# Optimization experiments

Hardware: AMD Instinct MI355X
Metric: run time of the kernel (lower is better)

The kernel has to match this reference:

```python
import jax, jax.numpy as jnp
import numpy as np

B = 1024
N_NODES = 30
E_PER = 82
IN_F = 128
HID = 256
HEADS = (3, 2, 1)
N_EH = 41


def _lin(k, fi, fo):
    s = 1.0 / np.sqrt(fi)
    kw, kb = jax.random.split(k)
    W = jax.random.uniform(kw, (fi, fo), jnp.float32, -s, s)
    b = jax.random.uniform(kb, (fo,), jnp.float32, -s, s)
    return W, b


def setup_inputs() -> dict:
    key = jax.random.key(0)
    ks = list(jax.random.split(key, 32))
    rng = np.random.default_rng(0)
    # base 30-node graph with E_PER directed edges, no self-loops
    src = rng.integers(0, N_NODES, E_PER)
    dst = (src + rng.integers(1, N_NODES, E_PER)) % N_NODES
    base = np.stack([src, dst])  # [2, E_PER]
    offs = (np.arange(B) * N_NODES)[None, None, :]  # [1,1,B]
    ei = (base[:, :, None] + offs).transpose(0, 2, 1).reshape(2, -1)  # [2, B*E_PER]
    e_h = rng.choice(E_PER, N_EH, replace=False)
    d = {}
    d["x"] = jax.random.normal(ks[0], (B * N_NODES, IN_F), jnp.float32)
    d["edge_index"] = jnp.asarray(ei, dtype=jnp.int32)
    d["e_h_pairs"] = jnp.asarray(base[:, e_h].T, dtype=jnp.int32)  # [N_EH, 2]
    d["Wp"], d["bp"] = _lin(ks[1], IN_F, HID)
    i = 2
    for l, H in enumerate(HEADS):
        d[f"ln_g{l}"] = jnp.ones((HID,), jnp.float32)
        d[f"ln_b{l}"] = jnp.zeros((HID,), jnp.float32)
        d[f"Wl{l}"], d[f"bl{l}"] = _lin(ks[i], HID, H * HID); i += 1
        d[f"Wr{l}"], d[f"br{l}"] = _lin(ks[i], HID, H * HID); i += 1
        d[f"att{l}"] = jax.random.normal(ks[i], (H, HID), jnp.float32) * 0.1; i += 1
        d[f"bias{l}"] = jnp.zeros((HID,), jnp.float32)
    dims = [2 * HID, 256, 128, 128, 1]
    for j in range(4):
        d[f"Wm{j}"], d[f"bm{j}"] = _lin(ks[i], dims[j], dims[j + 1]); i += 1
    return d


def _layer_norm(h, g, b):
    mu = jnp.mean(h, -1, keepdims=True)
    var = jnp.mean((h - mu) ** 2, -1, keepdims=True)
    return (h - mu) * jax.lax.rsqrt(var + 1e-5) * g + b


def _gatv2(h, src, dst, n, Wl, bl, Wr, br, att, bias):
    # PyG GATv2Conv, concat=False (mean over heads), self-loops already in src/dst
    H, C = att.shape
    xl = (h @ Wl + bl).reshape(-1, H, C)  # source transform
    xr = (h @ Wr + br).reshape(-1, H, C)  # target transform
    xj = xl[src]                          # [E,H,C]
    e = jax.nn.leaky_relu(xj + xr[dst], 0.2)
    logits = jnp.einsum('ehc,hc->eh', e, att)  # [E,H]
    m = jax.lax.stop_gradient(jax.ops.segment_max(logits, dst, num_segments=n))
    ex = jnp.exp(logits - m[dst])
    denom = jax.ops.segment_sum(ex, dst, num_segments=n)
    alpha = ex / denom[dst]               # softmax over incoming edges of dst
    out = jax.ops.segment_sum(xj * alpha[..., None], dst, num_segments=n)  # [N,H,C]
    return jnp.mean(out, 1) + bias


def reference(x, edge_index, e_h_pairs, Wp, bp,
              ln_g0, ln_b0, Wl0, bl0, Wr0, br0, att0, bias0,
              ln_g1, ln_b1, Wl1, bl1, Wr1, br1, att1, bias1,
              ln_g2, ln_b2, Wl2, bl2, Wr2, br2, att2, bias2,
              Wm0, bm0, Wm1, bm1, Wm2, bm2, Wm3, bm3):
    n = x.shape[0]
    loops = jnp.arange(n, dtype=edge_index.dtype)
    src = jnp.concatenate([edge_index[0], loops])
    dst = jnp.concatenate([edge_index[1], loops])
    lrelu = lambda v: jax.nn.leaky_relu(v, 0.01)
    h = x @ Wp + bp
    layers = [(ln_g0, ln_b0, Wl0, bl0, Wr0, br0, att0, bias0),
              (ln_g1, ln_b1, Wl1, bl1, Wr1, br1, att1, bias1),
              (ln_g2, ln_b2, Wl2, bl2, Wr2, br2, att2, bias2)]
    for (g, b, Wl, bl, Wr, br, att, bias) in layers:
        hn = _layer_norm(h, g, b)
        hc = _gatv2(hn, src, dst, n, Wl, bl, Wr, br, att, bias)
        h = lrelu(hc) + h  # dropout is identity in eval
    hb = h.reshape(-1, N_NODES, HID)  # [B, 30, 256]
    ef = jnp.concatenate([hb[:, e_h_pairs[:, 0], :], hb[:, e_h_pairs[:, 1], :]], -1)
    o = ef.reshape(-1, 2 * HID)
    o = lrelu(o @ Wm0 + bm0)
    o = lrelu(o @ Wm1 + bm1)
    o = lrelu(o @ Wm2 + bm2)
    o = o @ Wm3 + bm3
    return o.reshape(-1)
```

## Files before the change

### kernel.cpp

```cpp
#include <hip/hip_runtime.h>
#include <hip/hip_bf16.h>
#include <math.h>

#define N_NODES 30
#define E_BASE  82
#define E_TOT   112
#define B_GRAPH 1024
#define HID     256
#define NTOT    (B_GRAPH * N_NODES)
#define MAXIN   32
#define N_EH    41
#define M_MLP   (B_GRAPH * N_EH)

#define META_SRC  0
#define META_DST  E_TOT
#define META_CNT  (2 * E_TOT)
#define META_LIST 256
#define META_INTS 1216

typedef __attribute__((ext_vector_type(8))) short bf16x8;
typedef __attribute__((ext_vector_type(4))) short bf16x4;
typedef __attribute__((ext_vector_type(4))) float f32x4;
#define AS3 __attribute__((address_space(3)))
#define AS1 __attribute__((address_space(1)))

__device__ __forceinline__ void gload_lds16(const void* g, void* l) {
  __builtin_amdgcn_global_load_lds((const AS1 void*)g, (AS3 void*)l, 16, 0, 0);
}

__device__ __forceinline__ float b2f(short s) {
  union { unsigned u; float f; } x;
  x.u = ((unsigned)(unsigned short)s) << 16;
  return x.f;
}

__global__ void build_graph(const int* __restrict__ ei, int* __restrict__ meta) {
  __shared__ int cnt[N_NODES];
  int tid = threadIdx.x;
  if (tid < N_NODES) cnt[tid] = 0;
  __syncthreads();
  if (tid < E_TOT) {
    int s, d;
    if (tid < E_BASE) { s = ei[tid]; d = ei[B_GRAPH * E_BASE + tid]; }
    else              { s = tid - E_BASE; d = s; }
    meta[META_SRC + tid] = s;
    meta[META_DST + tid] = d;
    int pos = atomicAdd(&cnt[d], 1);
    if (pos < MAXIN) meta[META_LIST + d * MAXIN + pos] = tid;
  }
  __syncthreads();
  if (tid < N_NODES) meta[META_CNT + tid] = cnt[tid];
}

struct WtJob { const float* in; int K, N, tstart, ooff; };
struct WtArgs { WtJob j[10]; };

__global__ __launch_bounds__(256)
void transpose_weights(WtArgs args, __hip_bfloat16* __restrict__ out) {
  int b = blockIdx.x;
  int ji = 0;
  #pragma unroll
  for (int i = 1; i < 10; i++) if (b >= args.j[i].tstart) ji = i;
  WtJob jb = args.j[ji];
  int t = b - jb.tstart;
  int ntn = jb.N >> 5;
  int tk = t / ntn, tn = t - tk * ntn;
  int k0 = tk * 32, n0 = tn * 32;
  __shared__ float s[32][33];
  int tx = threadIdx.x & 31, ty = threadIdx.x >> 5;
  #pragma unroll
  for (int p = 0; p < 4; p++)
    s[ty + p * 8][tx] = jb.in[(size_t)(k0 + ty + p * 8) * jb.N + n0 + tx];
  __syncthreads();
  __hip_bfloat16* o = out + jb.ooff;
  #pragma unroll
  for (int p = 0; p < 4; p++) {
    int n = ty + p * 8;
    o[(size_t)(n0 + n) * jb.K + k0 + tx] = __float2bfloat16(s[tx][n]);
  }
}

template<int ACT, int OUTBF>
__global__ __launch_bounds__(256)
void gemm_mfma(const __hip_bfloat16* __restrict__ A, const __hip_bfloat16* __restrict__ Bt,
               const float* __restrict__ bias, const float* __restrict__ bias2,
               void* __restrict__ Cv, int M, int K, int N, int N1)
{
  __shared__ __hip_bfloat16 sA[128 * 32];
  __shared__ __hip_bfloat16 sB[128 * 32];
  const int tid = threadIdx.x;
  const int lane = tid & 63;
  const int wave = tid >> 6;
  const int wx = wave & 1, wy = wave >> 1;
  const int bm = blockIdx.x, bn = blockIdx.y;
  const int mrow = lane & 15, quad = lane >> 4;

  const int r0 = tid >> 2, kc0 = (tid & 3) * 8;
  const __hip_bfloat16* Ag0 = A + (size_t)(bm * 128 + r0) * K + kc0;
  const __hip_bfloat16* Ag1 = A + (size_t)(bm * 128 + r0 + 64) * K + kc0;
  const __hip_bfloat16* Bg0 = Bt + (size_t)(bn * 128 + r0) * K + kc0;
  const __hip_bfloat16* Bg1 = Bt + (size_t)(bn * 128 + r0 + 64) * K + kc0;

  f32x4 acc[4][4];
  #pragma unroll
  for (int i = 0; i < 4; i++)
    #pragma unroll
    for (int j = 0; j < 4; j++)
      acc[i][j] = (f32x4){0.f, 0.f, 0.f, 0.f};

  for (int kt = 0; kt < K; kt += 32) {
    __syncthreads();
    gload_lds16(Ag0 + kt, &sA[tid * 8]);
    gload_lds16(Ag1 + kt, &sA[2048 + tid * 8]);
    gload_lds16(Bg0 + kt, &sB[tid * 8]);
    gload_lds16(Bg1 + kt, &sB[2048 + tid * 8]);
    __syncthreads();

    bf16x8 af[4], bfr[4];
    #pragma unroll
    for (int i = 0; i < 4; i++) {
      af[i]  = *(const bf16x8*)&sA[(wy * 64 + i * 16 + mrow) * 32 + quad * 8];
      bfr[i] = *(const bf16x8*)&sB[(wx * 64 + i * 16 + mrow) * 32 + quad * 8];
    }
    #pragma unroll
    for (int i = 0; i < 4; i++)
      #pragma unroll
      for (int j = 0; j < 4; j++)
        acc[i][j] = __builtin_amdgcn_mfma_f32_16x16x32_bf16(af[i], bfr[j], acc[i][j], 0, 0, 0);
  }

  #pragma unroll
  for (int i = 0; i < 4; i++) {
    #pragma unroll
    for (int r = 0; r < 4; r++) {
      size_t row = (size_t)bm * 128 + wy * 64 + i * 16 + quad * 4 + r;
      #pragma unroll
      for (int j = 0; j < 4; j++) {
        int col = bn * 128 + wx * 64 + j * 16 + mrow;
        float bc = (col < N1) ? bias[col] : bias2[col - N1];
        float v = acc[i][j][r] + bc;
        if (ACT) v = v > 0.f ? v : 0.01f * v;
        if (OUTBF) ((__hip_bfloat16*)Cv)[row * N + col] = __float2bfloat16(v);
        else       ((float*)Cv)[row * N + col] = v;
      }
    }
  }
}

template<int ACT, int OUTBF>
__global__ __launch_bounds__(256)
void gemm_mfma_f32a(const float* __restrict__ A, const __hip_bfloat16* __restrict__ Bt,
                    const float* __restrict__ bias, void* __restrict__ Cv,
                    int M, int K, int N)
{
  __shared__ __hip_bfloat16 sA[128 * 32];
  __shared__ __hip_bfloat16 sB[128 * 32];
  const int tid = threadIdx.x;
  const int lane = tid & 63;
  const int wave = tid >> 6;
  const int wx = wave & 1, wy = wave >> 1;
  const int bm = blockIdx.x, bn = blockIdx.y;
  const int mrow = lane & 15, quad = lane >> 4;

  const int r0 = tid >> 2, kc0 = (tid & 3) * 8;
  const float* Ag0 = A + (size_t)(bm * 128 + r0) * K + kc0;
  const float* Ag1 = A + (size_t)(bm * 128 + r0 + 64) * K + kc0;
  const __hip_bfloat16* Bg0 = Bt + (size_t)(bn * 128 + r0) * K + kc0;
  const __hip_bfloat16* Bg1 = Bt + (size_t)(bn * 128 + r0 + 64) * K + kc0;

  f32x4 acc[4][4];
  #pragma unroll
  for (int i = 0; i < 4; i++)
    #pragma unroll
    for (int j = 0; j < 4; j++)
      acc[i][j] = (f32x4){0.f, 0.f, 0.f, 0.f};

  for (int kt = 0; kt < K; kt += 32) {
    float4 a00 = *(const float4*)(Ag0 + kt);
    float4 a01 = *(const float4*)(Ag0 + kt + 4);
    float4 a10 = *(const float4*)(Ag1 + kt);
    float4 a11 = *(const float4*)(Ag1 + kt + 4);
    __syncthreads();
    {
      __hip_bfloat16 t[8];
      t[0] = __float2bfloat16(a00.x); t[1] = __float2bfloat16(a00.y);
      t[2] = __float2bfloat16(a00.z); t[3] = __float2bfloat16(a00.w);
      t[4] = __float2bfloat16(a01.x); t[5] = __float2bfloat16(a01.y);
      t[6] = __float2bfloat16(a01.z); t[7] = __float2bfloat16(a01.w);
      *(bf16x8*)&sA[tid * 8] = *(bf16x8*)t;
      t[0] = __float2bfloat16(a10.x); t[1] = __float2bfloat16(a10.y);
      t[2] = __float2bfloat16(a10.z); t[3] = __float2bfloat16(a10.w);
      t[4] = __float2bfloat16(a11.x); t[5] = __float2bfloat16(a11.y);
      t[6] = __float2bfloat16(a11.z); t[7] = __float2bfloat16(a11.w);
      *(bf16x8*)&sA[2048 + tid * 8] = *(bf16x8*)t;
    }
    gload_lds16(Bg0 + kt, &sB[tid * 8]);
    gload_lds16(Bg1 + kt, &sB[2048 + tid * 8]);
    __syncthreads();

    bf16x8 af[4], bfr[4];
    #pragma unroll
    for (int i = 0; i < 4; i++) {
      af[i]  = *(const bf16x8*)&sA[(wy * 64 + i * 16 + mrow) * 32 + quad * 8];
      bfr[i] = *(const bf16x8*)&sB[(wx * 64 + i * 16 + mrow) * 32 + quad * 8];
    }
    #pragma unroll
    for (int i = 0; i < 4; i++)
      #pragma unroll
      for (int j = 0; j < 4; j++)
        acc[i][j] = __builtin_amdgcn_mfma_f32_16x16x32_bf16(af[i], bfr[j], acc[i][j], 0, 0, 0);
  }

  #pragma unroll
  for (int i = 0; i < 4; i++) {
    #pragma unroll
    for (int r = 0; r < 4; r++) {
      size_t row = (size_t)bm * 128 + wy * 64 + i * 16 + quad * 4 + r;
      #pragma unroll
      for (int j = 0; j < 4; j++) {
        int col = bn * 128 + wx * 64 + j * 16 + mrow;
        float v = acc[i][j][r] + bias[col];
        if (ACT) v = v > 0.f ? v : 0.01f * v;
        if (OUTBF) ((__hip_bfloat16*)Cv)[row * N + col] = __float2bfloat16(v);
        else       ((float*)Cv)[row * N + col] = v;
      }
    }
  }
}

__global__ __launch_bounds__(256)
void gemm_mfma_pair(const float* __restrict__ h, const int* __restrict__ pairs,
                    const __hip_bfloat16* __restrict__ Bt, const float* __restrict__ bias,
                    __hip_bfloat16* __restrict__ C, int N)
{
  const int K = 512;
  __shared__ __hip_bfloat16 sA[128 * 32];
  __shared__ __hip_bfloat16 sB[128 * 32];
  const int tid = threadIdx.x;
  const int lane = tid & 63;
  const int wave = tid >> 6;
  const int wx = wave & 1, wy = wave >> 1;
  const int bm = blockIdx.x, bn = blockIdx.y;
  const int mrow = lane & 15, quad = lane >> 4;

  const float* pu[2]; const float* pv[2]; int sub[2];
  #pragma unroll
  for (int cI = 0; cI < 2; cI++) {
    int c = tid + cI * 256;
    int r0 = c >> 2; sub[cI] = (c & 3) * 8;
    int R = bm * 128 + r0;
    int b = R / N_EH, p = R - b * N_EH;
    int u = pairs[p * 2], v = pairs[p * 2 + 1];
    pu[cI] = h + ((size_t)b * N_NODES + u) * HID;
    pv[cI] = h + ((size_t)b * N_NODES + v) * HID;
  }

  const int r0 = tid >> 2, kc0 = (tid & 3) * 8;
  const __hip_bfloat16* Bg0 = Bt + (size_t)(bn * 128 + r0) * K + kc0;
  const __hip_bfloat16* Bg1 = Bt + (size_t)(bn * 128 + r0 + 64) * K + kc0;

  f32x4 acc[4][4];
  #pragma unroll
  for (int i = 0; i < 4; i++)
    #pragma unroll
    for (int j = 0; j < 4; j++)
      acc[i][j] = (f32x4){0.f, 0.f, 0.f, 0.f};

  for (int kt = 0; kt < K; kt += 32) {
    float4 av[2][2];
    #pragma unroll
    for (int cI = 0; cI < 2; cI++) {
      const float* src = (kt < 256 ? pu[cI] + kt : pv[cI] + kt - 256) + sub[cI];
      av[cI][0] = *(const float4*)src;
      av[cI][1] = *(const float4*)(src + 4);
    }
    __syncthreads();
    #pragma unroll
    for (int cI = 0; cI < 2; cI++) {
      __hip_bfloat16 t[8];
      t[0] = __float2bfloat16(av[cI][0].x); t[1] = __float2bfloat16(av[cI][0].y);
      t[2] = __float2bfloat16(av[cI][0].z); t[3] = __float2bfloat16(av[cI][0].w);
      t[4] = __float2bfloat16(av[cI][1].x); t[5] = __float2bfloat16(av[cI][1].y);
      t[6] = __float2bfloat16(av[cI][1].z); t[7] = __float2bfloat16(av[cI][1].w);
      *(bf16x8*)&sA[(tid + cI * 256) * 8] = *(bf16x8*)t;
    }
    gload_lds16(Bg0 + kt, &sB[tid * 8]);
    gload_lds16(Bg1 + kt, &sB[2048 + tid * 8]);
    __syncthreads();

    bf16x8 af[4], bfr[4];
    #pragma unroll
    for (int i = 0; i < 4; i++) {
      af[i]  = *(const bf16x8*)&sA[(wy * 64 + i * 16 + mrow) * 32 + quad * 8];
      bfr[i] = *(const bf16x8*)&sB[(wx * 64 + i * 16 + mrow) * 32 + quad * 8];
    }
    #pragma unroll
    for (int i = 0; i < 4; i++)
      #pragma unroll
      for (int j = 0; j < 4; j++)
        acc[i][j] = __builtin_amdgcn_mfma_f32_16x16x32_bf16(af[i], bfr[j], acc[i][j], 0, 0, 0);
  }

  #pragma unroll
  for (int i = 0; i < 4; i++) {
    #pragma unroll
    for (int r = 0; r < 4; r++) {
      size_t row = (size_t)bm * 128 + wy * 64 + i * 16 + quad * 4 + r;
      #pragma unroll
      for (int j = 0; j < 4; j++) {
        int col = bn * 128 + wx * 64 + j * 16 + mrow;
        float v = acc[i][j][r] + bias[col];
        v = v > 0.f ? v : 0.01f * v;
        C[row * N + col] = __float2bfloat16(v);
      }
    }
  }
}

__global__ __launch_bounds__(256)
void layernorm(const float* __restrict__ h, const float* __restrict__ g,
               const float* __restrict__ b, __hip_bfloat16* __restrict__ hn)
{
  const int wv = threadIdx.x >> 6, lane = threadIdx.x & 63;
  const size_t row = (size_t)blockIdx.x * 4 + wv;
  const float* hr = h + row * HID;
  float v[4];
  float sum = 0.f;
  #pragma unroll
  for (int j = 0; j < 4; j++) { v[j] = hr[lane + 64 * j]; sum += v[j]; }
  #pragma unroll
  for (int off = 32; off; off >>= 1) sum += __shfl_xor(sum, off);
  float mu = sum * (1.f / 256.f);
  float vs = 0.f;
  #pragma unroll
  for (int j = 0; j < 4; j++) { float d = v[j] - mu; vs += d * d; }
  #pragma unroll
  for (int off = 32; off; off >>= 1) vs += __shfl_xor(vs, off);
  float rs = rsqrtf(vs * (1.f / 256.f) + 1e-5f);
  __hip_bfloat16* outr = hn + row * HID;
  #pragma unroll
  for (int j = 0; j < 4; j++) {
    int c = lane + 64 * j;
    outr[c] = __float2bfloat16((v[j] - mu) * rs * g[c] + b[c]);
  }
}

__global__ __launch_bounds__(256)
void gat_alpha(const __hip_bfloat16* __restrict__ xcat,
               const float* __restrict__ att, float* __restrict__ alphaG,
               const int* __restrict__ meta, int H)
{
  __shared__ __hip_bfloat16 sxl[N_NODES * HID];
  __shared__ __hip_bfloat16 sxr[N_NODES * HID];
  __shared__ float slog[E_TOT];
  __shared__ float smax[N_NODES];
  __shared__ float sden[N_NODES];
  __shared__ int ssrc[E_TOT], sdst[E_TOT], scnt[N_NODES], slist[N_NODES * MAXIN];

  const int tid = threadIdx.x;
  const int g = blockIdx.x, hh = blockIdx.y;
  const size_t nodebase = (size_t)g * N_NODES;
  const int S = 2 * H * HID;

  {
    int i = tid;
    #pragma unroll
    for (int p = 0; p < 4; p++, i += 256) {
      if (i < N_NODES * HID / 8) {
        int node = i >> 5, c = (i & 31) * 8;
        const __hip_bfloat16* row = &xcat[(nodebase + node) * S + c];
        gload_lds16(row + hh * HID, &sxl[(size_t)i * 8]);
        gload_lds16(row + (H + hh) * HID, &sxr[(size_t)i * 8]);
      }
    }
  }

  if (tid < E_TOT) { ssrc[tid] = meta[META_SRC + tid]; sdst[tid] = meta[META_DST + tid]; }
  if (tid < N_NODES) { scnt[tid] = meta[META_CNT + tid]; sden[tid] = 0.f; }
  for (int i = tid; i < N_NODES * MAXIN; i += 256) slist[i] = meta[META_LIST + i];

  const int wv = tid >> 6, l32 = tid & 31, esub = (tid >> 5) & 1;
  const int c0 = l32 * 8;
  float attr[8];
  #pragma unroll
  for (int j = 0; j < 8; j++) attr[j] = att[hh * HID + c0 + j];
  __syncthreads();

  #pragma unroll
  for (int pass = 0; pass < 14; pass++) {
    int e = pass * 8 + wv * 2 + esub;
    bf16x8 a = *(const bf16x8*)&sxl[ssrc[e] * HID + c0];
    bf16x8 b = *(const bf16x8*)&sxr[sdst[e] * HID + c0];
    float sum = 0.f;
    #pragma unroll
    for (int j = 0; j < 8; j++) {
      float v = b2f(a[j]) + b2f(b[j]);
      v = v > 0.f ? v : 0.2f * v;
      sum += v * attr[j];
    }
    #pragma unroll
    for (int off = 16; off; off >>= 1) sum += __shfl_xor(sum, off);
    if (l32 == 0) slog[e] = sum;
  }
  __syncthreads();

  if (tid < N_NODES) {
    int cnt = scnt[tid];
    const int* lst = &slist[tid * MAXIN];
    float m = -1e30f;
    for (int i = 0; i < cnt; i++) m = fmaxf(m, slog[lst[i]]);
    smax[tid] = m;
  }
  __syncthreads();
  if (tid < E_TOT) {
    float ex = expf(slog[tid] - smax[sdst[tid]]);
    slog[tid] = ex;
    atomicAdd(&sden[sdst[tid]], ex);
  }
  __syncthreads();
  if (tid < E_TOT)
    alphaG[((size_t)g * H + hh) * E_TOT + tid] = slog[tid] / sden[sdst[tid]];
}

template<int DO_LN>
__global__ __launch_bounds__(256, 4)
void gat_agg(const __hip_bfloat16* __restrict__ xcat, const float* __restrict__ alphaG,
             const float* __restrict__ bias, float* __restrict__ h,
             const float* __restrict__ lnG, const float* __restrict__ lnB,
             __hip_bfloat16* __restrict__ hn, const int* __restrict__ meta, int H)
{
  __shared__ __hip_bfloat16 sxl[2][N_NODES * HID];
  __shared__ float salpha[2][E_TOT];
  __shared__ int ssrc[E_TOT], scnt[N_NODES], slist[N_NODES * MAXIN];

  const int tid = threadIdx.x;
  const int g = blockIdx.x;
  const size_t nodebase = (size_t)g * N_NODES;
  const int S = 2 * H * HID;
  const int c4 = tid & 63;
  const int ng = tid >> 6;

  if (tid < E_TOT) ssrc[tid] = meta[META_SRC + tid];
  if (tid < N_NODES) scnt[tid] = meta[META_CNT + tid];
  for (int i = tid; i < N_NODES * MAXIN; i += 256) slist[i] = meta[META_LIST + i];

  float4 hres[8];
  #pragma unroll
  for (int ki = 0; ki < 8; ki++) {
    int k = ng + ki * 4;
    if (k < N_NODES) hres[ki] = *(const float4*)&h[(nodebase + k) * HID + c4 * 4];
  }

  {
    int i = tid;
    #pragma unroll
    for (int p = 0; p < 4; p++, i += 256) {
      if (i < N_NODES * HID / 8) {
        int node = i >> 5, c = (i & 31) * 8;
        gload_lds16(&xcat[(nodebase + node) * S + 0 * HID + c], &sxl[0][(size_t)i * 8]);
      }
    }
    if (tid < E_TOT) salpha[0][tid] = alphaG[((size_t)g * H + 0) * E_TOT + tid];
  }

  float acc[8][4];
  #pragma unroll
  for (int ki = 0; ki < 8; ki++)
    #pragma unroll
    for (int j = 0; j < 4; j++) acc[ki][j] = 0.f;

  for (int hh = 0; hh < H; hh++) {
    const int buf = hh & 1;
    __syncthreads();
    if (hh + 1 < H) {
      const int nb = buf ^ 1;
      int i = tid;
      #pragma unroll
      for (int p = 0; p < 4; p++, i += 256) {
        if (i < N_NODES * HID / 8) {
          int node = i >> 5, c = (i & 31) * 8;
          gload_lds16(&xcat[(nodebase + node) * S + (hh + 1) * HID + c], &sxl[nb][(size_t)i * 8]);
        }
      }
      if (tid < E_TOT) salpha[nb][tid] = alphaG[((size_t)g * H + hh + 1) * E_TOT + tid];
    }
    #pragma unroll
    for (int ki = 0; ki < 8; ki++) {
      int k = ng + ki * 4;
      if (k < N_NODES) {
        int cnt = scnt[k];
        const int* lst = &slist[k * MAXIN];
        for (int i = 0; i < cnt; i++) {
          int e = lst[i];
          float al = salpha[buf][e];
          bf16x4 v = *(const bf16x4*)&sxl[buf][ssrc[e] * HID + c4 * 4];
          acc[ki][0] += al * b2f(v[0]);
          acc[ki][1] += al * b2f(v[1]);
          acc[ki][2] += al * b2f(v[2]);
          acc[ki][3] += al * b2f(v[3]);
        }
      }
    }
  }

  const float invH = 1.f / (float)H;
  const float4 bs = *(const float4*)&bias[c4 * 4];
  float4 gv, bv;
  if (DO_LN) {
    gv = *(const float4*)&lnG[c4 * 4];
    bv = *(const float4*)&lnB[c4 * 4];
  }
  #pragma unroll
  for (int ki = 0; ki < 8; ki++) {
    int k = ng + ki * 4;
    if (k < N_NODES) {
      float o0 = acc[ki][0] * invH + bs.x; o0 = o0 > 0.f ? o0 : 0.01f * o0; o0 += hres[ki].x;
      float o1 = acc[ki][1] * invH + bs.y; o1 = o1 > 0.f ? o1 : 0.01f * o1; o1 += hres[ki].y;
      float o2 = acc[ki][2] * invH + bs.z; o2 = o2 > 0.f ? o2 : 0.01f * o2; o2 += hres[ki].z;
      float o3 = acc[ki][3] * invH + bs.w; o3 = o3 > 0.f ? o3 : 0.01f * o3; o3 += hres[ki].w;
      float4 o4 = {o0, o1, o2, o3};
      *(float4*)&h[(nodebase + k) * HID + c4 * 4] = o4;
      if (DO_LN) {
        float sum = o0 + o1 + o2 + o3;
        #pragma unroll
        for (int off = 32; off; off >>= 1) sum += __shfl_xor(sum, off);
        float mu = sum * (1.f / 256.f);
        float d0 = o0 - mu, d1 = o1 - mu, d2 = o2 - mu, d3 = o3 - mu;
        float vs = d0 * d0 + d1 * d1 + d2 * d2 + d3 * d3;
        #pragma unroll
        for (int off = 32; off; off >>= 1) vs += __shfl_xor(vs, off);
        float rs = rsqrtf(vs * (1.f / 256.f) + 1e-5f);
        __hip_bfloat16 t[4];
        t[0] = __float2bfloat16(d0 * rs * gv.x + bv.x);
        t[1] = __float2bfloat16(d1 * rs * gv.y + bv.y);
        t[2] = __float2bfloat16(d2 * rs * gv.z + bv.z);
        t[3] = __float2bfloat16(d3 * rs * gv.w + bv.w);
        *(bf16x4*)&hn[(nodebase + k) * HID + c4 * 4] = *(bf16x4*)t;
      }
    }
  }
}

__global__ __launch_bounds__(256)
void mlp_out(const float* __restrict__ o3, const float* __restrict__ w,
             const float* __restrict__ b3, float* __restrict__ out)
{
  const int wv = threadIdx.x >> 6, lane = threadIdx.x & 63;
  const int row = blockIdx.x * 4 + wv;
  const float* orow = o3 + (size_t)row * 128;
  float s = orow[lane] * w[lane] + orow[lane + 64] * w[lane + 64];
  #pragma unroll
  for (int off = 32; off; off >>= 1) s += __shfl_xor(s, off);
  if (lane == 0) out[row] = s + b3[0];
}

extern "C" void kernel_launch(void* const* d_in, const int* in_sizes, int n_in,
                              void* d_out, int out_size, void* d_ws, size_t ws_size,
                              hipStream_t stream) {
  const float* x     = (const float*)d_in[0];
  const int*   ei    = (const int*)d_in[1];
  const int*   pairs = (const int*)d_in[2];
  const float* bp    = (const float*)d_in[4];
  const float *lng[3], *lnb[3], *bl[3], *br[3], *att[3], *bias[3];
  const float *WlF[3], *WrF[3];
  for (int l = 0; l < 3; l++) {
    int base = 5 + l * 8;
    lng[l]  = (const float*)d_in[base + 0];
    lnb[l]  = (const float*)d_in[base + 1];
    WlF[l]  = (const float*)d_in[base + 2];
    bl[l]   = (const float*)d_in[base + 3];
    WrF[l]  = (const float*)d_in[base + 4];
    br[l]   = (const float*)d_in[base + 5];
    att[l]  = (const float*)d_in[base + 6];
    bias[l] = (const float*)d_in[base + 7];
  }
  const float* WmF[4] = {(const float*)d_in[29], (const float*)d_in[31],
                         (const float*)d_in[33], (const float*)d_in[35]};
  const float* bm[4] = {(const float*)d_in[30], (const float*)d_in[32],
                        (const float*)d_in[34], (const float*)d_in[36]};

  float* ws  = (float*)d_ws;
  float* h   = ws;
  __hip_bfloat16* hnb = (__hip_bfloat16*)(ws + 7864320);
  __hip_bfloat16* xcat = (__hip_bfloat16*)(ws + 11796480);
  float* alphaG = ws + 35389440;
  __hip_bfloat16* wbuf = (__hip_bfloat16*)(ws + 35733504);
  int*   meta = (int*)(ws + 36233216);
  __hip_bfloat16* o1b = (__hip_bfloat16*)xcat;
  __hip_bfloat16* o2b = (__hip_bfloat16*)(ws + 17170432);
  float* o3 = ws + 23592960;
  float* out = (float*)d_out;

  const int oWp = 0, oWl0 = 32768, oWr0 = 229376, oWl1 = 425984, oWr1 = 557056;
  const int oWl2 = 688128, oWr2 = 753664, oWm0 = 819200, oWm1 = 950272, oWm2 = 983040;

  build_graph<<<1, 128, 0, stream>>>(ei, meta);

  WtArgs wa;
  wa.j[0] = {(const float*)d_in[3], 128, 256,   0, oWp };
  wa.j[1] = {WlF[0],              256, 768,  32, oWl0};
  wa.j[2] = {WrF[0],              256, 768, 224, oWr0};
  wa.j[3] = {WlF[1],              256, 512, 416, oWl1};
  wa.j[4] = {WrF[1],              256, 512, 544, oWr1};
  wa.j[5] = {WlF[2],              256, 256, 672, oWl2};
  wa.j[6] = {WrF[2],              256, 256, 736, oWr2};
  wa.j[7] = {WmF[0],              512, 256, 800, oWm0};
  wa.j[8] = {WmF[1],              256, 128, 928, oWm1};
  wa.j[9] = {WmF[2],              128, 128, 960, oWm2};
  transpose_weights<<<976, 256, 0, stream>>>(wa, wbuf);

  gemm_mfma_f32a<0, 0><<<dim3(NTOT / 128, 2), 256, 0, stream>>>(x, wbuf + oWp, bp, h,
                                                                NTOT, 128, 256);

  layernorm<<<NTOT / 4, 256, 0, stream>>>(h, lng[0], lnb[0], hnb);

  const int Hs[3] = {3, 2, 1};
  const int oWl[3] = {oWl0, oWl1, oWl2};
  for (int l = 0; l < 3; l++) {
    int N = 2 * Hs[l] * HID;
    gemm_mfma<0, 1><<<dim3(NTOT / 128, N / 128), 256, 0, stream>>>(
        hnb, wbuf + oWl[l], bl[l], br[l], xcat, NTOT, HID, N, N / 2);
    gat_alpha<<<dim3(B_GRAPH, Hs[l]), 256, 0, stream>>>(xcat, att[l], alphaG, meta, Hs[l]);
    if (l < 2)
      gat_agg<1><<<B_GRAPH, 256, 0, stream>>>(xcat, alphaG, bias[l], h,
                                              lng[l + 1], lnb[l + 1], hnb, meta, Hs[l]);
    else
      gat_agg<0><<<B_GRAPH, 256, 0, stream>>>(xcat, alphaG, bias[l], h,
                                              nullptr, nullptr, nullptr, meta, Hs[l]);
  }

  gemm_mfma_pair<<<dim3(M_MLP / 128, 2), 256, 0, stream>>>(h, pairs, wbuf + oWm0, bm[0], o1b, 256);
  gemm_mfma<1, 1><<<dim3(M_MLP / 128, 1), 256, 0, stream>>>(o1b, wbuf + oWm1, bm[1], bm[1], o2b,
                                                            M_MLP, 256, 128, 128);
  gemm_mfma<1, 0><<<dim3(M_MLP / 128, 1), 256, 0, stream>>>(o2b, wbuf + oWm2, bm[2], bm[2], o3,
                                                            M_MLP, 128, 128, 128);
  mlp_out<<<M_MLP / 4, 256, 0, stream>>>(o3, WmF[3], bm[3], out);
}
```

Before: 456.4 us.

## Fuse MLP tail layers into one kernel and fold graph build into transpose

```diff
diff --git a/kernel.cpp b/kernel.cpp
--- a/kernel.cpp
+++ b/kernel.cpp
@@ -34,30 +34,31 @@
   return x.f;
 }
 
-__global__ void build_graph(const int* __restrict__ ei, int* __restrict__ meta) {
-  __shared__ int cnt[N_NODES];
-  int tid = threadIdx.x;
-  if (tid < N_NODES) cnt[tid] = 0;
-  __syncthreads();
-  if (tid < E_TOT) {
-    int s, d;
-    if (tid < E_BASE) { s = ei[tid]; d = ei[B_GRAPH * E_BASE + tid]; }
-    else              { s = tid - E_BASE; d = s; }
-    meta[META_SRC + tid] = s;
-    meta[META_DST + tid] = d;
-    int pos = atomicAdd(&cnt[d], 1);
-    if (pos < MAXIN) meta[META_LIST + d * MAXIN + pos] = tid;
-  }
-  __syncthreads();
-  if (tid < N_NODES) meta[META_CNT + tid] = cnt[tid];
-}
-
 struct WtJob { const float* in; int K, N, tstart, ooff; };
 struct WtArgs { WtJob j[10]; };
 
 __global__ __launch_bounds__(256)
-void transpose_weights(WtArgs args, __hip_bfloat16* __restrict__ out) {
+void transpose_weights(WtArgs args, __hip_bfloat16* __restrict__ out,
+                       const int* __restrict__ ei, int* __restrict__ meta) {
   int b = blockIdx.x;
+  if (b == 976) {
+    __shared__ int cnt[N_NODES];
+    int tid = threadIdx.x;
+    if (tid < N_NODES) cnt[tid] = 0;
+    __syncthreads();
+    if (tid < E_TOT) {
+      int s, d;
+      if (tid < E_BASE) { s = ei[tid]; d = ei[B_GRAPH * E_BASE + tid]; }
+      else              { s = tid - E_BASE; d = s; }
+      meta[META_SRC + tid] = s;
+      meta[META_DST + tid] = d;
+      int pos = atomicAdd(&cnt[d], 1);
+      if (pos < MAXIN) meta[META_LIST + d * MAXIN + pos] = tid;
+    }
+    __syncthreads();
+    if (tid < N_NODES) meta[META_CNT + tid] = cnt[tid];
+    return;
+  }
   int ji = 0;
   #pragma unroll
   for (int i = 1; i < 10; i++) if (b >= args.j[i].tstart) ji = i;
@@ -315,6 +316,131 @@
       }
     }
   }
+}
+
+#define O2P 136
+__global__ __launch_bounds__(256)
+void mlp_tail(const __hip_bfloat16* __restrict__ o1, const __hip_bfloat16* __restrict__ W1t,
+              const float* __restrict__ b1, const __hip_bfloat16* __restrict__ W2t,
+              const float* __restrict__ b2, const float* __restrict__ w3,
+              const float* __restrict__ b3, float* __restrict__ out)
+{
+  __shared__ __hip_bfloat16 sA[128 * 32];
+  __shared__ __hip_bfloat16 sB[128 * 32];
+  __shared__ __hip_bfloat16 sO2[128 * O2P];
+  __shared__ float spart[2][128];
+  const int tid = threadIdx.x;
+  const int lane = tid & 63;
+  const int wave = tid >> 6;
+  const int wx = wave & 1, wy = wave >> 1;
+  const int bm = blockIdx.x;
+  const int mrow = lane & 15, quad = lane >> 4;
+  const int r0 = tid >> 2, kc0 = (tid & 3) * 8;
+
+  const __hip_bfloat16* Ag0 = o1 + (size_t)(bm * 128 + r0) * 256 + kc0;
+  const __hip_bfloat16* Ag1 = o1 + (size_t)(bm * 128 + r0 + 64) * 256 + kc0;
+  const __hip_bfloat16* Bg0 = W1t + (size_t)r0 * 256 + kc0;
+  const __hip_bfloat16* Bg1 = W1t + (size_t)(r0 + 64) * 256 + kc0;
+
+  f32x4 acc[4][4];
+  #pragma unroll
+  for (int i = 0; i < 4; i++)
+    #pragma unroll
+    for (int j = 0; j < 4; j++)
+      acc[i][j] = (f32x4){0.f, 0.f, 0.f, 0.f};
+
+  for (int kt = 0; kt < 256; kt += 32) {
+    __syncthreads();
+    gload_lds16(Ag0 + kt, &sA[tid * 8]);
+    gload_lds16(Ag1 + kt, &sA[2048 + tid * 8]);
+    gload_lds16(Bg0 + kt, &sB[tid * 8]);
+    gload_lds16(Bg1 + kt, &sB[2048 + tid * 8]);
+    __syncthreads();
+
+    bf16x8 af[4], bfr[4];
+    #pragma unroll
+    for (int i = 0; i < 4; i++) {
+      af[i]  = *(const bf16x8*)&sA[(wy * 64 + i * 16 + mrow) * 32 + quad * 8];
+      bfr[i] = *(const bf16x8*)&sB[(wx * 64 + i * 16 + mrow) * 32 + quad * 8];
+    }
+    #pragma unroll
+    for (int i = 0; i < 4; i++)
+      #pragma unroll
+      for (int j = 0; j < 4; j++)
+        acc[i][j] = __builtin_amdgcn_mfma_f32_16x16x32_bf16(af[i], bfr[j], acc[i][j], 0, 0, 0);
+  }
+
+  __syncthreads();
+  #pragma unroll
+  for (int i = 0; i < 4; i++) {
+    #pragma unroll
+    for (int r = 0; r < 4; r++) {
+      int row = wy * 64 + i * 16 + quad * 4 + r;
+      #pragma unroll
+      for (int j = 0; j < 4; j++) {
+        int col = wx * 64 + j * 16 + mrow;
+        float v = acc[i][j][r] + b1[col];
+        v = v > 0.f ? v : 0.01f * v;
+        sO2[row * O2P + col] = __float2bfloat16(v);
+      }
+    }
+  }
+
+  f32x4 acc2[4][4];
+  #pragma unroll
+  for (int i = 0; i < 4; i++)
+    #pragma unroll
+    for (int j = 0; j < 4; j++)
+      acc2[i][j] = (f32x4){0.f, 0.f, 0.f, 0.f};
+
+  for (int kt = 0; kt < 128; kt += 32) {
+    __syncthreads();
+    gload_lds16(W2t + (size_t)r0 * 128 + kt + kc0, &sB[tid * 8]);
+    gload_lds16(W2t + (size_t)(r0 + 64) * 128 + kt + kc0, &sB[2048 + tid * 8]);
+    __syncthreads();
+
+    bf16x8 af[4], bfr[4];
+    #pragma unroll
+    for (int i = 0; i < 4; i++) {
+      af[i]  = *(const bf16x8*)&sO2[(wy * 64 + i * 16 + mrow) * O2P + kt + quad * 8];
+      bfr[i] = *(const bf16x8*)&sB[(wx * 64 + i * 16 + mrow) * 32 + quad * 8];
+    }
+    #pragma unroll
+    for (int i = 0; i < 4; i++)
+      #pragma unroll
+      for (int j = 0; j < 4; j++)
+        acc2[i][j] = __builtin_amdgcn_mfma_f32_16x16x32_bf16(af[i], bfr[j], acc2[i][j], 0, 0, 0);
+  }
+
+  float w3v[4], b2v[4];
+  #pragma unroll
+  for (int j = 0; j < 4; j++) {
+    int col = wx * 64 + j * 16 + mrow;
+    w3v[j] = w3[col];
+    b2v[j] = b2[col];
+  }
+  #pragma unroll
+  for (int i = 0; i < 4; i++) {
+    #pragma unroll
+    for (int r = 0; r < 4; r++) {
+      float s = 0.f;
+      #pragma unroll
+      for (int j = 0; j < 4; j++) {
+        float v = acc2[i][j][r] + b2v[j];
+        v = v > 0.f ? v : 0.01f * v;
+        s += v * w3v[j];
+      }
+      #pragma unroll
+      for (int off = 8; off; off >>= 1) s += __shfl_xor(s, off);
+      if (mrow == 0) {
+        int row = wy * 64 + i * 16 + quad * 4 + r;
+        spart[wx][row] = s;
+      }
+    }
+  }
+  __syncthreads();
+  if (tid < 128)
+    out[(size_t)bm * 128 + tid] = spart[0][tid] + spart[1][tid] + b3[0];
 }
 
 __global__ __launch_bounds__(256)
@@ -541,19 +667,6 @@
   }
 }
 
-__global__ __launch_bounds__(256)
-void mlp_out(const float* __restrict__ o3, const float* __restrict__ w,
-             const float* __restrict__ b3, float* __restrict__ out)
-{
-  const int wv = threadIdx.x >> 6, lane = threadIdx.x & 63;
-  const int row = blockIdx.x * 4 + wv;
-  const float* orow = o3 + (size_t)row * 128;
-  float s = orow[lane] * w[lane] + orow[lane + 64] * w[lane + 64];
-  #pragma unroll
-  for (int off = 32; off; off >>= 1) s += __shfl_xor(s, off);
-  if (lane == 0) out[row] = s + b3[0];
-}
-
 extern "C" void kernel_launch(void* const* d_in, const int* in_sizes, int n_in,
                               void* d_out, int out_size, void* d_ws, size_t ws_size,
                               hipStream_t stream) {
@@ -587,14 +700,10 @@
   __hip_bfloat16* wbuf = (__hip_bfloat16*)(ws + 35733504);
   int*   meta = (int*)(ws + 36233216);
   __hip_bfloat16* o1b = (__hip_bfloat16*)xcat;
-  __hip_bfloat16* o2b = (__hip_bfloat16*)(ws + 17170432);
-  float* o3 = ws + 23592960;
   float* out = (float*)d_out;
 
   const int oWp = 0, oWl0 = 32768, oWr0 = 229376, oWl1 = 425984, oWr1 = 557056;
   const int oWl2 = 688128, oWr2 = 753664, oWm0 = 819200, oWm1 = 950272, oWm2 = 983040;
-
-  build_graph<<<1, 128, 0, stream>>>(ei, meta);
 
   WtArgs wa;
   wa.j[0] = {(const float*)d_in[3], 128, 256,   0, oWp };
@@ -607,7 +716,7 @@
   wa.j[7] = {WmF[0],              512, 256, 800, oWm0};
   wa.j[8] = {WmF[1],              256, 128, 928, oWm1};
   wa.j[9] = {WmF[2],              128, 128, 960, oWm2};
-  transpose_weights<<<976, 256, 0, stream>>>(wa, wbuf);
+  transpose_weights<<<977, 256, 0, stream>>>(wa, wbuf, ei, meta);
 
   gemm_mfma_f32a<0, 0><<<dim3(NTOT / 128, 2), 256, 0, stream>>>(x, wbuf + oWp, bp, h,
                                                                 NTOT, 128, 256);
@@ -630,9 +739,6 @@
   }
 
   gemm_mfma_pair<<<dim3(M_MLP / 128, 2), 256, 0, stream>>>(h, pairs, wbuf + oWm0, bm[0], o1b, 256);
-  gemm_mfma<1, 1><<<dim3(M_MLP / 128, 1), 256, 0, stream>>>(o1b, wbuf + oWm1, bm[1], bm[1], o2b,
-                                                            M_MLP, 256, 128, 128);
-  gemm_mfma<1, 0><<<dim3(M_MLP / 128, 1), 256, 0, stream>>>(o2b, wbuf + oWm2, bm[2], bm[2], o3,
-                                                            M_MLP, 128, 128, 128);
-  mlp_out<<<M_MLP / 4, 256, 0, stream>>>(o3, WmF[3], bm[3], out);
-}
+  mlp_tail<<<M_MLP / 128, 256, 0, stream>>>(o1b, wbuf + oWm1, bm[1], wbuf + oWm2, bm[2],
+                                            WmF[3], bm[3], out);
+}
```

After: 443.6 us. 1.03x faster.
